# Performance work log

Hardware: AMD Instinct MI355X
Metric: run time of the kernel (lower is better)

The kernel has to match this reference:

```python
import jax, jax.numpy as jnp
import numpy as np

H = 16          # n_heads
EPS = 1e-3      # keras LayerNormalization default epsilon


def _layernorm(x, gamma, beta):
    m = jnp.mean(x, axis=-1, keepdims=True)
    v = jnp.var(x, axis=-1, keepdims=True)
    return (x - m) * jax.lax.rsqrt(v + EPS) * gamma + beta


def _mha(q, k, v, wq, bq, wk, bk, wv, bv, wo, bo, causal):
    B, Sq, D = q.shape
    Sk = k.shape[1]
    d = D // H
    qh = (q @ wq + bq).reshape(B, Sq, H, d)
    kh = (k @ wk + bk).reshape(B, Sk, H, d)
    vh = (v @ wv + bv).reshape(B, Sk, H, d)
    scores = jnp.einsum('bqhd,bkhd->bhqk', qh, kh) / jnp.sqrt(jnp.asarray(d, qh.dtype))
    if causal:
        mask = jnp.tril(jnp.ones((Sq, Sk), dtype=bool))
        scores = jnp.where(mask, scores, jnp.asarray(-1e9, scores.dtype))
    attn = jax.nn.softmax(scores, axis=-1)
    out = jnp.einsum('bhqk,bkhd->bqhd', attn, vh).reshape(B, Sq, D)
    return out @ wo + bo


def setup_inputs() -> dict:
    key = jax.random.key(0)
    B, S, D, DFF = 4, 1024, 1024, 4096
    ks = jax.random.split(key, 16)
    sc = 0.02
    inp = {
        'inputs': jax.random.normal(ks[0], (B, S, D), jnp.float32),
        'enc_outputs': jax.random.normal(ks[1], (B, S, D), jnp.float32),
    }
    # self-attention (mha1)
    inp['wq1'] = jax.random.normal(ks[2], (D, D), jnp.float32) * sc
    inp['wk1'] = jax.random.normal(ks[3], (D, D), jnp.float32) * sc
    inp['wv1'] = jax.random.normal(ks[4], (D, D), jnp.float32) * sc
    inp['wo1'] = jax.random.normal(ks[5], (D, D), jnp.float32) * sc
    inp['bq1'] = jnp.zeros((D,), jnp.float32)
    inp['bk1'] = jnp.zeros((D,), jnp.float32)
    inp['bv1'] = jnp.zeros((D,), jnp.float32)
    inp['bo1'] = jnp.zeros((D,), jnp.float32)
    # cross-attention (mha2)
    inp['wq2'] = jax.random.normal(ks[6], (D, D), jnp.float32) * sc
    inp['wk2'] = jax.random.normal(ks[7], (D, D), jnp.float32) * sc
    inp['wv2'] = jax.random.normal(ks[8], (D, D), jnp.float32) * sc
    inp['wo2'] = jax.random.normal(ks[9], (D, D), jnp.float32) * sc
    inp['bq2'] = jnp.zeros((D,), jnp.float32)
    inp['bk2'] = jnp.zeros((D,), jnp.float32)
    inp['bv2'] = jnp.zeros((D,), jnp.float32)
    inp['bo2'] = jnp.zeros((D,), jnp.float32)
    # FFN
    inp['w_ff1'] = jax.random.normal(ks[10], (D, DFF), jnp.float32) * sc
    inp['b_ff1'] = jnp.zeros((DFF,), jnp.float32)
    inp['w_ff2'] = jax.random.normal(ks[11], (DFF, D), jnp.float32) * sc
    inp['b_ff2'] = jnp.zeros((D,), jnp.float32)
    # LayerNorms
    for i in (1, 2, 3):
        inp[f'g{i}'] = jnp.ones((D,), jnp.float32)
        inp[f'be{i}'] = jnp.zeros((D,), jnp.float32)
    return inp


def reference(inputs, enc_outputs,
              wq1, bq1, wk1, bk1, wv1, bv1, wo1, bo1,
              wq2, bq2, wk2, bk2, wv2, bv2, wo2, bo2,
              w_ff1, b_ff1, w_ff2, b_ff2,
              g1, be1, g2, be2, g3, be3):
    # self-attention block (causal) + residual + LN; dropout is identity (eval)
    a1 = _mha(inputs, inputs, inputs, wq1, bq1, wk1, bk1, wv1, bv1, wo1, bo1, causal=True)
    o1 = _layernorm(inputs + a1, g1, be1)
    # cross-attention block + residual + LN
    a2 = _mha(o1, enc_outputs, enc_outputs, wq2, bq2, wk2, bk2, wv2, bv2, wo2, bo2, causal=False)
    o2 = _layernorm(o1 + a2, g2, be2)
    # FFN block + residual + LN
    f = jax.nn.relu(o2 @ w_ff1 + b_ff1) @ w_ff2 + b_ff2
    return _layernorm(o2 + f, g3, be3)
```

## Files before the change

kernel.cpp:

```cpp
#include <hip/hip_runtime.h>
#include <stdint.h>
#include <stddef.h>

typedef __attribute__((ext_vector_type(4))) float  floatx4;
typedef __attribute__((ext_vector_type(8))) short  short8;
typedef __attribute__((ext_vector_type(4))) short  short4v;

__device__ __forceinline__ float bf2f(short s) {
  union { uint32_t u; float f; } v;
  v.u = ((uint32_t)(uint16_t)s) << 16;
  return v.f;
}
__device__ __forceinline__ short f2bf(float f) {
  union { float f; uint32_t u; } v; v.f = f;
  uint32_t r = v.u + 0x7fffu + ((v.u >> 16) & 1u);
  return (short)(r >> 16);
}

__device__ __forceinline__ void async_cp16(const void* g, void* l) {
  __builtin_amdgcn_global_load_lds(
      (__attribute__((address_space(1))) void*)g,
      (__attribute__((address_space(3))) void*)l, 16, 0, 0);
}

#define WAITB(N) do {                                        \
  asm volatile("s_waitcnt vmcnt(" #N ")" ::: "memory");      \
  __builtin_amdgcn_s_barrier();                              \
  __builtin_amdgcn_sched_barrier(0); } while (0)

__device__ __forceinline__ int swzb(int row, int bcol) {
  return ((row << 7) + bcol) ^ ((row & 7) << 4);
}

struct TransTable {
  const float* src[10];
  short*       dst[10];
  int K[10], N[10], base[10];
};
__global__ __launch_bounds__(256)
void transpose_all(TransTable tt)
{
  __shared__ short tile[32][33];
  int e = 0;
  #pragma unroll
  for (int i = 1; i < 10; i++) if ((int)blockIdx.x >= tt.base[i]) e = i;
  const int t = blockIdx.x - tt.base[e];
  const int N = tt.N[e], K = tt.K[e];
  const int ncols = N >> 5;
  const int n0 = (t % ncols) << 5, k0 = (t / ncols) << 5;
  const float* src = tt.src[e];
  short* dst = tt.dst[e];
  const int tx = threadIdx.x & 31, ty = threadIdx.x >> 5;
  #pragma unroll
  for (int i = 0; i < 32; i += 8)
    tile[ty + i][tx] = f2bf(src[(size_t)(k0 + ty + i) * N + n0 + tx]);
  __syncthreads();
  #pragma unroll
  for (int i = 0; i < 32; i += 8)
    dst[(size_t)(n0 + ty + i) * K + k0 + tx] = tile[tx][ty + i];
}

__global__ __launch_bounds__(256)
void convert_xe(const float* __restrict__ x, const float* __restrict__ enc,
                short* __restrict__ xc, short* __restrict__ encc)
{
  int b = blockIdx.x;
  const float* s; short* d;
  if (b < 4096) { s = x; d = xc; } else { s = enc; d = encc; b -= 4096; }
  const int i = (b * 256 + threadIdx.x) * 4;
  const floatx4 v = *(const floatx4*)(s + i);
  short4v o;
  #pragma unroll
  for (int j = 0; j < 4; j++) o[j] = f2bf(v[j]);
  *(short4v*)(d + i) = o;
}

struct ParamMap { const float* s[19]; int off[19]; };
__global__ __launch_bounds__(256)
void convert_params(ParamMap pm, short* __restrict__ dst)
{
  const int b = blockIdx.x;
  for (int t = threadIdx.x; t < 1024; t += 256)
    dst[b * 1024 + t] = f2bf(pm.s[b][pm.off[b] + t]);
}

template<int RELU, int RESID, int BM, int BN>
__global__ __launch_bounds__(256)
void gemm_bt(const short* __restrict__ A, const short* __restrict__ BT,
             const short* __restrict__ bias, const short* __restrict__ resid,
             short* __restrict__ C, int M, int N, int K)
{
  constexpr int MT = BM / 32;
  constexpr int NT = BN / 32;
  __shared__ short8 As0[BM * 4];
  __shared__ short8 As1[BM * 4];
  __shared__ short8 Bs0[BN * 4];
  __shared__ short8 Bs1[BN * 4];
  const int tid  = threadIdx.x;
  const int w    = tid >> 6;
  const int lane = tid & 63;
  const int m16  = lane & 15;
  const int g    = lane >> 4;
  const int nbn  = N / BN;
  const int bid  = ((int)blockIdx.x & 7) * ((int)gridDim.x >> 3) + ((int)blockIdx.x >> 3);
  const int bm   = bid / nbn;
  const int bn   = bid % nbn;
  const int wm   = (w >> 1) * (BM / 2);
  const int wn   = (w & 1) * (BN / 2);

  const int r0 = lane >> 2;
  const int c0 = lane & 3;
  const int csw = c0 ^ ((r0 >> 1) & 3);
  const short* pA = A  + (size_t)(bm * BM + w * (BM / 4) + r0) * K + csw * 8;
  const short* pB = BT + (size_t)(bn * BN + w * (BN / 4) + r0) * K + csw * 8;

  floatx4 acc[MT][NT];
  #pragma unroll
  for (int i = 0; i < MT; i++)
    #pragma unroll
    for (int j = 0; j < NT; j++)
      acc[i][j] = floatx4{0.f, 0.f, 0.f, 0.f};

  auto stage = [&](short8* AS, short8* BS, int k0) {
    async_cp16(pA + k0, AS + w * BM);
    if constexpr (BM == 128) async_cp16(pA + k0 + 16 * (size_t)K, AS + w * BM + 64);
    async_cp16(pB + k0, BS + w * BN);
    if constexpr (BN == 128) async_cp16(pB + k0 + 16 * (size_t)K, BS + w * BN + 64);
  };
  const int gs = g ^ ((m16 >> 1) & 3);
  auto compute = [&](const short8* AS, const short8* BS) {
    short8 af[MT], bfr[NT];
    #pragma unroll
    for (int mt = 0; mt < MT; mt++)
      af[mt] = AS[(wm + mt * 16 + m16) * 4 + gs];
    #pragma unroll
    for (int nt = 0; nt < NT; nt++)
      bfr[nt] = BS[(wn + nt * 16 + m16) * 4 + gs];
    #pragma unroll
    for (int mt = 0; mt < MT; mt++)
      #pragma unroll
      for (int nt = 0; nt < NT; nt++)
        acc[mt][nt] = __builtin_amdgcn_mfma_f32_16x16x32_bf16(af[mt], bfr[nt], acc[mt][nt], 0, 0, 0);
  };

  stage(As0, Bs0, 0);
  __syncthreads();

  for (int k0 = 0; k0 < K; k0 += 64) {
    stage(As1, Bs1, k0 + 32);
    compute(As0, Bs0);
    __syncthreads();
    if (k0 + 64 < K)
      stage(As0, Bs0, k0 + 64);
    compute(As1, Bs1);
    __syncthreads();
  }

  #pragma unroll
  for (int mt = 0; mt < MT; mt++) {
    const int rbase = bm * BM + wm + mt * 16 + g * 4;
    #pragma unroll
    for (int nt = 0; nt < NT; nt++) {
      const int col = bn * BN + wn + nt * 16 + m16;
      const float bia = bf2f(bias[col]);
      #pragma unroll
      for (int r = 0; r < 4; r++) {
        const size_t idx = (size_t)(rbase + r) * N + col;
        float v = acc[mt][nt][r] + bia;
        if (RESID) v += bf2f(resid[idx]);
        if (RELU)  v = fmaxf(v, 0.f);
        C[idx] = f2bf(v);
      }
    }
  }
}

template<int RELU, int RESID>
__global__ __launch_bounds__(256)
void gemm_bt64(const short* __restrict__ A, const short* __restrict__ BT,
               const short* __restrict__ bias, const short* __restrict__ resid,
               short* __restrict__ C, int M, int N, int K)
{
  __shared__ short8 As0[256], As1[256], As2[256], As3[256];
  __shared__ short8 Bs0[256], Bs1[256], Bs2[256], Bs3[256];
  const int tid  = threadIdx.x;
  const int w    = tid >> 6;
  const int lane = tid & 63;
  const int m16  = lane & 15;
  const int g    = lane >> 4;
  const int nbn  = N >> 6;
  const int bid  = ((int)blockIdx.x & 7) * ((int)gridDim.x >> 3) + ((int)blockIdx.x >> 3);
  const int bm   = bid / nbn;
  const int bn   = bid % nbn;
  const int wm   = (w >> 1) << 5;
  const int wn   = (w & 1) << 5;

  const int r0 = lane >> 2;
  const int c0 = lane & 3;
  const int csw = c0 ^ ((r0 >> 1) & 3);
  const short* pA = A  + (size_t)(bm * 64 + w * 16 + r0) * K + csw * 8;
  const short* pB = BT + (size_t)(bn * 64 + w * 16 + r0) * K + csw * 8;

  floatx4 acc[2][2];
  #pragma unroll
  for (int i = 0; i < 2; i++)
    #pragma unroll
    for (int j = 0; j < 2; j++)
      acc[i][j] = floatx4{0.f, 0.f, 0.f, 0.f};

  auto stage = [&](short8* AS, short8* BS, int k0) {
    async_cp16(pA + k0, AS + w * 64);
    async_cp16(pB + k0, BS + w * 64);
  };
  const int gs = g ^ ((m16 >> 1) & 3);
  auto compute = [&](const short8* AS, const short8* BS) {
    short8 af[2], bfr[2];
    #pragma unroll
    for (int mt = 0; mt < 2; mt++)
      af[mt] = AS[(wm + mt * 16 + m16) * 4 + gs];
    #pragma unroll
    for (int nt = 0; nt < 2; nt++)
      bfr[nt] = BS[(wn + nt * 16 + m16) * 4 + gs];
    #pragma unroll
    for (int mt = 0; mt < 2; mt++)
      #pragma unroll
      for (int nt = 0; nt < 2; nt++)
        acc[mt][nt] = __builtin_amdgcn_mfma_f32_16x16x32_bf16(af[mt], bfr[nt], acc[mt][nt], 0, 0, 0);
  };

  stage(As0, Bs0, 0);
  stage(As1, Bs1, 32);

  int k0 = 0;
  for (; k0 + 256 <= K; k0 += 128) {
    stage(As2, Bs2, k0 + 64);  WAITB(4); compute(As0, Bs0);
    stage(As3, Bs3, k0 + 96);  WAITB(4); compute(As1, Bs1);
    stage(As0, Bs0, k0 + 128); WAITB(4); compute(As2, Bs2);
    stage(As1, Bs1, k0 + 160); WAITB(4); compute(As3, Bs3);
  }
  stage(As2, Bs2, k0 + 64);  WAITB(4); compute(As0, Bs0);
  stage(As3, Bs3, k0 + 96);  WAITB(4); compute(As1, Bs1);
  WAITB(2); compute(As2, Bs2);
  WAITB(0); compute(As3, Bs3);

  #pragma unroll
  for (int mt = 0; mt < 2; mt++) {
    const int rbase = bm * 64 + wm + mt * 16 + g * 4;
    #pragma unroll
    for (int nt = 0; nt < 2; nt++) {
      const int col = bn * 64 + wn + nt * 16 + m16;
      const float bia = bf2f(bias[col]);
      #pragma unroll
      for (int r = 0; r < 4; r++) {
        const size_t idx = (size_t)(rbase + r) * N + col;
        float v = acc[mt][nt][r] + bia;
        if (RESID) v += bf2f(resid[idx]);
        if (RELU)  v = fmaxf(v, 0.f);
        C[idx] = f2bf(v);
      }
    }
  }
}

template<int CAUSAL>
__global__ __launch_bounds__(256, 4)
void attention(const short* __restrict__ Qp, int ldq,
               const short* __restrict__ Kp, int ldk,
               const short* __restrict__ Vp, int ldv,
               short* __restrict__ Op, int ldo)
{
  const int S   = 1024;
  const int bid = blockIdx.x;
  const int qt  = bid & 15;
  const int h   = (bid >> 4) & 15;
  const int b   = bid >> 8;
  const int tid = threadIdx.x;
  const int w   = tid >> 6;
  const int lane = tid & 63;
  const int m16 = lane & 15;
  const int g   = lane >> 4;

  __shared__ __align__(16) short Ks[2][64 * 64];
  __shared__ __align__(16) short VT[2][64 * 64];
  __shared__ __align__(16) short Ps[4][16 * 64];

  const int rowQ = b * S + qt * 64;
  const int wrow = w * 16;

  const short* qsrc = Qp + (size_t)(rowQ + wrow + m16) * ldq + h * 64 + 8 * g;
  const short8 qf0 = *(const short8*)qsrc;
  const short8 qf1 = *(const short8*)(qsrc + 32);

  float mrow = -1e38f;
  float lrow = 0.f;
  floatx4 oacc[4];
  #pragma unroll
  for (int dt = 0; dt < 4; dt++) oacc[dt] = floatx4{0.f, 0.f, 0.f, 0.f};

  const int kr  = tid >> 2, kc = (tid & 3) << 4;
  const int vkp = (tid & 31) * 2, vcg = (tid >> 5) << 3;

  const short* kbase = Kp + (size_t)(b * S + kr)  * ldk + h * 64 + kc;
  const short* vbase = Vp + (size_t)(b * S + vkp) * ldv + h * 64 + vcg;

  const int nkt = CAUSAL ? (qt + 1) : (S / 64);
  const int qi  = qt * 64 + wrow + m16;

  short8 kst0 = *(const short8*)kbase;
  short8 kst1 = *(const short8*)(kbase + 8);
  short8 vst0 = *(const short8*)vbase;
  short8 vst1 = *(const short8*)(vbase + ldv);
  {
    char* kd = (char*)&Ks[0][0];
    *(short8*)(kd + swzb(kr, kc * 2))      = kst0;
    *(short8*)(kd + swzb(kr, kc * 2 + 16)) = kst1;
    char* vd = (char*)&VT[0][0];
    #pragma unroll
    for (int j = 0; j < 8; j++) {
      const uint32_t pk = (uint32_t)(uint16_t)vst0[j] | ((uint32_t)(uint16_t)vst1[j] << 16);
      *(uint32_t*)(vd + swzb(vcg + j, vkp * 2)) = pk;
    }
  }
  __syncthreads();

  for (int kt = 0; kt < nkt; kt++) {
    const int cur  = kt & 1;
    const int more = (kt + 1 < nkt);

    if (more) {
      const size_t roff = (size_t)(kt + 1) * 64;
      kst0 = *(const short8*)(kbase + roff * ldk);
      kst1 = *(const short8*)(kbase + roff * ldk + 8);
      vst0 = *(const short8*)(vbase + roff * ldv);
      vst1 = *(const short8*)(vbase + roff * ldv + ldv);
    }

    const int kb = kt * 64;

    const char* ksrc = (const char*)&Ks[cur][0];
    floatx4 sc[4];
    #pragma unroll
    for (int cg4 = 0; cg4 < 4; cg4++) {
      const short8 kfa = *(const short8*)(ksrc + swzb(cg4 * 16 + m16, 16 * g));
      const short8 kfb = *(const short8*)(ksrc + swzb(cg4 * 16 + m16, 64 + 16 * g));
      sc[cg4] = __builtin_amdgcn_mfma_f32_16x16x32_bf16(kfa, qf0, floatx4{0.f,0.f,0.f,0.f}, 0, 0, 0);
      sc[cg4] = __builtin_amdgcn_mfma_f32_16x16x32_bf16(kfb, qf1, sc[cg4], 0, 0, 0);
    }

    float v4[4][4];
    #pragma unroll
    for (int cg = 0; cg < 4; cg++)
      #pragma unroll
      for (int r = 0; r < 4; r++) {
        float x = sc[cg][r] * 0.125f;
        if (CAUSAL && kt == qt) {
          const int key = kb + cg * 16 + g * 4 + r;
          if (key > qi) x = -1e9f;
        }
        v4[cg][r] = x;
      }

    float mx = v4[0][0];
    #pragma unroll
    for (int cg = 0; cg < 4; cg++)
      #pragma unroll
      for (int r = 0; r < 4; r++) mx = fmaxf(mx, v4[cg][r]);
    mx = fmaxf(mx, __shfl_xor(mx, 16));
    mx = fmaxf(mx, __shfl_xor(mx, 32));
    const float mn = fmaxf(mrow, mx);
    const float alpha = __expf(mrow - mn);
    mrow = mn;

    float rs = 0.f;
    #pragma unroll
    for (int cg = 0; cg < 4; cg++)
      #pragma unroll
      for (int r = 0; r < 4; r++) { v4[cg][r] = __expf(v4[cg][r] - mn); rs += v4[cg][r]; }
    rs += __shfl_xor(rs, 16);
    rs += __shfl_xor(rs, 32);
    lrow = lrow * alpha + rs;

    #pragma unroll
    for (int r = 0; r < 4; r++) {
      const float aR = __shfl(alpha, (g << 2) | r);
      #pragma unroll
      for (int dt = 0; dt < 4; dt++) oacc[dt][r] *= aR;
    }

    char* pbase = (char*)&Ps[w][0];
    #pragma unroll
    for (int cg = 0; cg < 4; cg++) {
      const uint32_t p0 = (uint32_t)(uint16_t)f2bf(v4[cg][0]) |
                          ((uint32_t)(uint16_t)f2bf(v4[cg][1]) << 16);
      const uint32_t p1 = (uint32_t)(uint16_t)f2bf(v4[cg][2]) |
                          ((uint32_t)(uint16_t)f2bf(v4[cg][3]) << 16);
      *(uint32_t*)(pbase + swzb(m16, (8 * cg + 2 * g) * 4))     = p0;
      *(uint32_t*)(pbase + swzb(m16, (8 * cg + 2 * g + 1) * 4)) = p1;
    }

    asm volatile("s_waitcnt lgkmcnt(0)" ::: "memory");
    __builtin_amdgcn_sched_barrier(0);

    const short8 pf0 = *(const short8*)(pbase + swzb(m16, 16 * g));
    const short8 pf1 = *(const short8*)(pbase + swzb(m16, 64 + 16 * g));
    const char* vsrc = (const char*)&VT[cur][0];
    #pragma unroll
    for (int dt = 0; dt < 4; dt++) {
      const short8 vfa = *(const short8*)(vsrc + swzb(dt * 16 + m16, 16 * g));
      const short8 vfb = *(const short8*)(vsrc + swzb(dt * 16 + m16, 64 + 16 * g));
      oacc[dt] = __builtin_amdgcn_mfma_f32_16x16x32_bf16(pf0, vfa, oacc[dt], 0, 0, 0);
      oacc[dt] = __builtin_amdgcn_mfma_f32_16x16x32_bf16(pf1, vfb, oacc[dt], 0, 0, 0);
    }

    if (more) {
      char* kd = (char*)&Ks[cur ^ 1][0];
      *(short8*)(kd + swzb(kr, kc * 2))      = kst0;
      *(short8*)(kd + swzb(kr, kc * 2 + 16)) = kst1;
      char* vd = (char*)&VT[cur ^ 1][0];
      #pragma unroll
      for (int j = 0; j < 8; j++) {
        const uint32_t pk = (uint32_t)(uint16_t)vst0[j] | ((uint32_t)(uint16_t)vst1[j] << 16);
        *(uint32_t*)(vd + swzb(vcg + j, vkp * 2)) = pk;
      }
      __syncthreads();
    }
  }

  float lR[4];
  #pragma unroll
  for (int r = 0; r < 4; r++) lR[r] = __shfl(lrow, (g << 2) | r);
  #pragma unroll
  for (int dt = 0; dt < 4; dt++)
    #pragma unroll
    for (int r = 0; r < 4; r++) {
      const size_t orow = (size_t)(rowQ + wrow + g * 4 + r);
      Op[orow * ldo + h * 64 + dt * 16 + m16] = f2bf(oacc[dt][r] / lR[r]);
    }
}

template<int FINAL>
__global__ __launch_bounds__(256)
void layernorm_bf16(const short* __restrict__ x, const short* __restrict__ gamma,
                    const short* __restrict__ beta, void* __restrict__ out)
{
  const int D = 1024;
  const int row = blockIdx.x, tid = threadIdx.x;
  const short* xr = x + (size_t)row * D;
  short4v xv = *(const short4v*)(xr + tid * 4);
  float v[4], s = 0.f, ss = 0.f;
  #pragma unroll
  for (int j = 0; j < 4; j++) { v[j] = bf2f(xv[j]); s += v[j]; ss += v[j] * v[j]; }
  #pragma unroll
  for (int off = 32; off; off >>= 1) { s += __shfl_xor(s, off); ss += __shfl_xor(ss, off); }
  __shared__ float red[8];
  const int w = tid >> 6, lane = tid & 63;
  if (lane == 0) { red[w] = s; red[4 + w] = ss; }
  __syncthreads();
  s  = red[0] + red[1] + red[2] + red[3];
  ss = red[4] + red[5] + red[6] + red[7];
  const float mean = s * (1.f / D);
  const float var  = ss * (1.f / D) - mean * mean;
  const float inv  = rsqrtf(var + 1e-3f);
  float o[4];
  #pragma unroll
  for (int j = 0; j < 4; j++)
    o[j] = (v[j] - mean) * inv * bf2f(gamma[tid * 4 + j]) + bf2f(beta[tid * 4 + j]);
  if (FINAL) {
    floatx4 ov;
    #pragma unroll
    for (int j = 0; j < 4; j++) ov[j] = o[j];
    *(floatx4*)((float*)out + (size_t)row * D + tid * 4) = ov;
  } else {
    short4v ov;
    #pragma unroll
    for (int j = 0; j < 4; j++) ov[j] = f2bf(o[j]);
    *(short4v*)((short*)out + (size_t)row * D + tid * 4) = ov;
  }
}

extern "C" void kernel_launch(void* const* d_in, const int* in_sizes, int n_in,
                              void* d_out, int out_size, void* d_ws, size_t ws_size,
                              hipStream_t stream) {
  (void)in_sizes; (void)n_in; (void)out_size; (void)ws_size;
  const int M = 4096;
  const size_t MM = 1024 * 1024;

  short* ws = (short*)d_ws;
  short* wt_qkv1 = ws;
  short* wt_o1   = wt_qkv1 + 3 * MM;
  short* wt_q2   = wt_o1 + MM;
  short* wt_kv2  = wt_q2 + MM;
  short* wt_o2   = wt_kv2 + 2 * MM;
  short* wt_ff1  = wt_o2 + MM;
  short* wt_ff2  = wt_ff1 + 4 * MM;
  short* P       = ws + 16 * MM;
  short* encc    = ws + 16 * MM + 32768;
  short* act0    = encc + 4 * MM;
  short* attn    = act0 + 16 * MM;
  short* t1      = attn + 4 * MM;
  short* t2      = t1 + 4 * MM;
  short* xc      = t2;

  short* bqkv1 = P,        *bo1  = P + 3072, *bkv2 = P + 4096, *bq2 = P + 6144;
  short* bo2   = P + 7168, *bff1 = P + 8192, *bff2 = P + 12288;
  short* g1 = P + 13312, *be1 = P + 14336, *g2 = P + 15360, *be2 = P + 16384;
  short* g3 = P + 17408, *be3 = P + 18432;

  ParamMap pm;
  const int srcidx[19] = {6, 7, 8, 9, 15, 16, 14, 17, 19, 19, 19, 19, 21, 22, 23, 24, 25, 26, 27};
  const int offs[19]   = {0, 0, 0, 0, 0,  0,  0,  0,  0, 1024, 2048, 3072, 0, 0, 0, 0, 0, 0, 0};
  for (int i = 0; i < 19; i++) { pm.s[i] = (const float*)d_in[srcidx[i]]; pm.off[i] = offs[i]; }
  convert_params<<<19, 256, 0, stream>>>(pm, P);

  convert_xe<<<8192, 256, 0, stream>>>((const float*)d_in[0], (const float*)d_in[1], xc, encc);

  TransTable tt;
  const int widx[10] = {2, 3, 4, 5, 10, 11, 12, 13, 18, 20};
  short* wdst[10] = {wt_qkv1, wt_qkv1 + MM, wt_qkv1 + 2 * MM, wt_o1, wt_q2,
                     wt_kv2, wt_kv2 + MM, wt_o2, wt_ff1, wt_ff2};
  const int wK[10] = {1024, 1024, 1024, 1024, 1024, 1024, 1024, 1024, 1024, 4096};
  const int wN[10] = {1024, 1024, 1024, 1024, 1024, 1024, 1024, 1024, 4096, 1024};
  int base = 0;
  for (int i = 0; i < 10; i++) {
    tt.src[i] = (const float*)d_in[widx[i]];
    tt.dst[i] = wdst[i];
    tt.K[i] = wK[i]; tt.N[i] = wN[i]; tt.base[i] = base;
    base += (wN[i] / 32) * (wK[i] / 32);
  }
  transpose_all<<<base, 256, 0, stream>>>(tt);

  short* qkv1 = act0;
  gemm_bt<0, 0, 128, 128><<<dim3((M / 128) * (3072 / 128)), 256, 0, stream>>>(
      xc, wt_qkv1, bqkv1, nullptr, qkv1, M, 3072, 1024);
  attention<1><<<dim3(1024), 256, 0, stream>>>(
      qkv1, 3072, qkv1 + 1024, 3072, qkv1 + 2048, 3072, attn, 1024);
  gemm_bt64<0, 1><<<dim3((M / 64) * (1024 / 64)), 256, 0, stream>>>(
      attn, wt_o1, bo1, xc, t1, M, 1024, 1024);
  layernorm_bf16<0><<<dim3(4096), 256, 0, stream>>>(t1, g1, be1, t1);

  short* kv2 = act0;
  short* q2  = act0 + 8 * MM;
  gemm_bt<0, 0, 64, 128><<<dim3((M / 64) * (2048 / 128)), 256, 0, stream>>>(
      encc, wt_kv2, bkv2, nullptr, kv2, M, 2048, 1024);
  gemm_bt64<0, 0><<<dim3((M / 64) * (1024 / 64)), 256, 0, stream>>>(
      t1, wt_q2, bq2, nullptr, q2, M, 1024, 1024);
  attention<0><<<dim3(1024), 256, 0, stream>>>(
      q2, 1024, kv2, 2048, kv2 + 1024, 2048, attn, 1024);
  gemm_bt64<0, 1><<<dim3((M / 64) * (1024 / 64)), 256, 0, stream>>>(
      attn, wt_o2, bo2, t1, t2, M, 1024, 1024);
  layernorm_bf16<0><<<dim3(4096), 256, 0, stream>>>(t2, g2, be2, t2);

  short* hidden = act0;
  gemm_bt<1, 0, 128, 128><<<dim3((M / 128) * (4096 / 128)), 256, 0, stream>>>(
      t2, wt_ff1, bff1, nullptr, hidden, M, 4096, 1024);
  gemm_bt64<0, 1><<<dim3((M / 64) * (1024 / 64)), 256, 0, stream>>>(
      hidden, wt_ff2, bff2, t2, attn, M, 1024, 4096);
  layernorm_bf16<1><<<dim3(4096), 256, 0, stream>>>(attn, g3, be3, d_out);
}
```

Before: 522.0 us.

## Use two-stage 64-wide K tiles with __syncthreads in gemm_bt64

Replaces the four-buffer 32-wide K pipeline with explicit vmcnt waits by a double-buffered 64-wide K pipeline that uses __syncthreads. Each stage now loads two 16-byte chunks per operand per thread, and the LDS swizzle changes to an 8-column XOR pattern. The aim is fewer barriers per K step and larger tiles per sync. In exchange, prefetch depth is shallower, and relying on __syncthreads alone to wait for the async global-to-LDS loads may not guarantee completion.

Result: faster. 498.7 us (-4.5%).

```diff
diff --git a/kernel.cpp b/kernel.cpp
--- a/kernel.cpp
+++ b/kernel.cpp
@@ -22,11 +22,6 @@
       (__attribute__((address_space(1))) void*)g,
       (__attribute__((address_space(3))) void*)l, 16, 0, 0);
 }
-
-#define WAITB(N) do {                                        \
-  asm volatile("s_waitcnt vmcnt(" #N ")" ::: "memory");      \
-  __builtin_amdgcn_s_barrier();                              \
-  __builtin_amdgcn_sched_barrier(0); } while (0)
 
 __device__ __forceinline__ int swzb(int row, int bcol) {
   return ((row << 7) + bcol) ^ ((row & 7) << 4);
@@ -181,8 +176,8 @@
                const short* __restrict__ bias, const short* __restrict__ resid,
                short* __restrict__ C, int M, int N, int K)
 {
-  __shared__ short8 As0[256], As1[256], As2[256], As3[256];
-  __shared__ short8 Bs0[256], Bs1[256], Bs2[256], Bs3[256];
+  __shared__ short8 As0[512], As1[512];
+  __shared__ short8 Bs0[512], Bs1[512];
   const int tid  = threadIdx.x;
   const int w    = tid >> 6;
   const int lane = tid & 63;
@@ -195,9 +190,9 @@
   const int wm   = (w >> 1) << 5;
   const int wn   = (w & 1) << 5;
 
-  const int r0 = lane >> 2;
-  const int c0 = lane & 3;
-  const int csw = c0 ^ ((r0 >> 1) & 3);
+  const int r0  = lane >> 3;
+  const int c0  = lane & 7;
+  const int csw = c0 ^ r0;
   const short* pA = A  + (size_t)(bm * 64 + w * 16 + r0) * K + csw * 8;
   const short* pB = BT + (size_t)(bn * 64 + w * 16 + r0) * K + csw * 8;
 
@@ -209,39 +204,43 @@
       acc[i][j] = floatx4{0.f, 0.f, 0.f, 0.f};
 
   auto stage = [&](short8* AS, short8* BS, int k0) {
-    async_cp16(pA + k0, AS + w * 64);
-    async_cp16(pB + k0, BS + w * 64);
+    async_cp16(pA + k0,                 AS + w * 128);
+    async_cp16(pA + k0 + 8 * (size_t)K, AS + w * 128 + 64);
+    async_cp16(pB + k0,                 BS + w * 128);
+    async_cp16(pB + k0 + 8 * (size_t)K, BS + w * 128 + 64);
   };
-  const int gs = g ^ ((m16 >> 1) & 3);
+  const int sw = m16 & 7;
   auto compute = [&](const short8* AS, const short8* BS) {
-    short8 af[2], bfr[2];
-    #pragma unroll
-    for (int mt = 0; mt < 2; mt++)
-      af[mt] = AS[(wm + mt * 16 + m16) * 4 + gs];
-    #pragma unroll
-    for (int nt = 0; nt < 2; nt++)
-      bfr[nt] = BS[(wn + nt * 16 + m16) * 4 + gs];
-    #pragma unroll
-    for (int mt = 0; mt < 2; mt++)
+    #pragma unroll
+    for (int s = 0; s < 2; s++) {
+      const int pc = (4 * s + g) ^ sw;
+      short8 af[2], bfr[2];
+      #pragma unroll
+      for (int mt = 0; mt < 2; mt++)
+        af[mt] = AS[(wm + mt * 16 + m16) * 8 + pc];
       #pragma unroll
       for (int nt = 0; nt < 2; nt++)
-        acc[mt][nt] = __builtin_amdgcn_mfma_f32_16x16x32_bf16(af[mt], bfr[nt], acc[mt][nt], 0, 0, 0);
+        bfr[nt] = BS[(wn + nt * 16 + m16) * 8 + pc];
+      #pragma unroll
+      for (int mt = 0; mt < 2; mt++)
+        #pragma unroll
+        for (int nt = 0; nt < 2; nt++)
+          acc[mt][nt] = __builtin_amdgcn_mfma_f32_16x16x32_bf16(af[mt], bfr[nt], acc[mt][nt], 0, 0, 0);
+    }
   };
 
   stage(As0, Bs0, 0);
-  stage(As1, Bs1, 32);
-
-  int k0 = 0;
-  for (; k0 + 256 <= K; k0 += 128) {
-    stage(As2, Bs2, k0 + 64);  WAITB(4); compute(As0, Bs0);
-    stage(As3, Bs3, k0 + 96);  WAITB(4); compute(As1, Bs1);
-    stage(As0, Bs0, k0 + 128); WAITB(4); compute(As2, Bs2);
-    stage(As1, Bs1, k0 + 160); WAITB(4); compute(As3, Bs3);
-  }
-  stage(As2, Bs2, k0 + 64);  WAITB(4); compute(As0, Bs0);
-  stage(As3, Bs3, k0 + 96);  WAITB(4); compute(As1, Bs1);
-  WAITB(2); compute(As2, Bs2);
-  WAITB(0); compute(As3, Bs3);
+  __syncthreads();
+
+  for (int k0 = 0; k0 < K; k0 += 128) {
+    stage(As1, Bs1, k0 + 64);
+    compute(As0, Bs0);
+    __syncthreads();
+    if (k0 + 128 < K)
+      stage(As0, Bs0, k0 + 128);
+    compute(As1, Bs1);
+    __syncthreads();
+  }
 
   #pragma unroll
   for (int mt = 0; mt < 2; mt++) {
```
